# Kernel tuning notes

Hardware: AMD Instinct MI355X
Metric: run time of the kernel (lower is better)

## Reference

```python
import jax, jax.numpy as jnp
import numpy as np

NODE_DIM, HIDDEN_DIM, OUT_DIM = 64, 128, 64
N_NODES, N_EDGES = 50000, 800000
SLOPE = 0.05


def leaky(x):
    return jnp.where(x >= 0, x, SLOPE * x)


def setup_inputs() -> dict:
    key = jax.random.key(0)
    ks = jax.random.split(key, 8)
    x = jax.random.normal(ks[0], (N_NODES, NODE_DIM), dtype=jnp.float32)
    edge_index = jax.random.randint(ks[1], (2, N_EDGES), 0, N_NODES, dtype=jnp.int64)
    s0 = 1.0 / np.sqrt(NODE_DIM)
    s1 = 1.0 / np.sqrt(HIDDEN_DIM)
    W0 = jax.random.uniform(ks[2], (NODE_DIM, HIDDEN_DIM), jnp.float32, -s0, s0)
    b0 = jax.random.uniform(ks[3], (HIDDEN_DIM,), jnp.float32, -s0, s0)
    W1 = jax.random.uniform(ks[4], (HIDDEN_DIM, HIDDEN_DIM), jnp.float32, -s1, s1)
    b1 = jax.random.uniform(ks[5], (HIDDEN_DIM,), jnp.float32, -s1, s1)
    W2 = jax.random.uniform(ks[6], (HIDDEN_DIM, OUT_DIM), jnp.float32, -s1, s1)
    b2 = jax.random.uniform(ks[7], (OUT_DIM,), jnp.float32, -s1, s1)
    return {"x": x, "edge_index": edge_index, "W0": W0, "b0": b0,
            "W1": W1, "b1": b1, "W2": W2, "b2": b2}


def reference(x, edge_index, W0, b0, W1, b1, W2, b2):
    # gather-sum: [E, node_dim]
    e = x[edge_index[0]] + x[edge_index[1]]
    h = leaky(e @ W0 + b0)          # [E, hidden]
    h = leaky(h @ W1 + b1)          # [E, hidden]
    out = leaky(h @ W2 + b2)        # [E, out]
    return out
```

## Files before the change

kernel.cpp:

```cpp
#include <hip/hip_runtime.h>

typedef _Float16 half8  __attribute__((ext_vector_type(8)));
typedef float    floatx4 __attribute__((ext_vector_type(4)));

#define N_NODES 50000
#define N_EDGES 800000
#define SLOPE 0.05f

#define WS_XH  0ull
#define WS_W0  (WS_XH + (size_t)N_NODES * 64 * 2)
#define WS_W1  (WS_W0 + 128 * 64 * 2)
#define WS_W2  (WS_W1 + 128 * 128 * 2)
#define WS_B0  (WS_W2 + 64 * 128 * 2)
#define WS_B1  (WS_B0 + 128 * 4)
#define WS_B2  (WS_B1 + 128 * 4)

#define HC_STRIDE 40
#define XCONV_BLOCKS 782
#define PREP_BLOCKS (XCONV_BLOCKS + 65)

__device__ __forceinline__ float leaky(float t) { return t >= 0.f ? t : SLOPE * t; }

__global__ void prep_kernel(const float* __restrict__ x,
                            const float* __restrict__ W0, const float* __restrict__ W1,
                            const float* __restrict__ W2, const float* __restrict__ b0,
                            const float* __restrict__ b1, const float* __restrict__ b2,
                            unsigned char* __restrict__ ws) {
    const int b = blockIdx.x;
    if (b < XCONV_BLOCKS) {
        _Float16* xh = (_Float16*)(ws + WS_XH);
        const int i = (b * 512 + threadIdx.x) * 8;
        if (i < N_NODES * 64) {
            floatx4 u0 = *(const floatx4*)(x + i);
            floatx4 u1 = *(const floatx4*)(x + i + 4);
            half8 h;
            #pragma unroll
            for (int j = 0; j < 4; ++j) { h[j] = (_Float16)u0[j]; h[4 + j] = (_Float16)u1[j]; }
            *(half8*)(xh + i) = h;
        }
        return;
    }
    const int t = (b - XCONV_BLOCKS) * 512 + threadIdx.x;
    _Float16* w0t = (_Float16*)(ws + WS_W0);
    _Float16* wt1 = (_Float16*)(ws + WS_W1);
    _Float16* wt2 = (_Float16*)(ws + WS_W2);
    if (t < 8192) {
        int k = t >> 7, n = t & 127;
        w0t[n * 64 + k] = (_Float16)W0[k * 128 + n];
    } else if (t < 24576) {
        int i2 = t - 8192, k = i2 >> 7, n = i2 & 127;
        wt1[n * 128 + k] = (_Float16)W1[k * 128 + n];
    } else if (t < 32768) {
        int i2 = t - 24576, k = i2 >> 6, n = i2 & 63;
        wt2[n * 128 + k] = (_Float16)W2[k * 64 + n];
    } else if (t < 33088) {
        int i2 = t - 32768;
        if (i2 < 128) ((float*)(ws + WS_B0))[i2] = b0[i2];
        else if (i2 < 256) ((float*)(ws + WS_B1))[i2 - 128] = b1[i2 - 128];
        else ((float*)(ws + WS_B2))[i2 - 256] = b2[i2 - 256];
    }
}

__global__ __launch_bounds__(512, 4) void edge_kernel(const int* __restrict__ ei,
                                                      const unsigned char* __restrict__ ws,
                                                      float* __restrict__ out) {
    __shared__ __align__(16) _Float16 w0s[128 * 64];
    __shared__ __align__(16) _Float16 w1s[128 * 128];
    __shared__ __align__(16) _Float16 w2s[64 * 128];
    __shared__ __align__(16) _Float16 hc[8][16 * HC_STRIDE];
    __shared__ __align__(16) float b0s[128], b1s[128], b2s[64];

    const _Float16* __restrict__ xh  = (const _Float16*)(ws + WS_XH);
    const _Float16* __restrict__ w0g = (const _Float16*)(ws + WS_W0);
    const _Float16* __restrict__ w1g = (const _Float16*)(ws + WS_W1);
    const _Float16* __restrict__ w2g = (const _Float16*)(ws + WS_W2);

    const int wave = threadIdx.x >> 6, lane = threadIdx.x & 63;
    const int cl = lane & 15, q = lane >> 4;
    const int base = blockIdx.x * 256 + wave * 32;

    const int r0 = base + cl;
    const int s0 = ei[r0], d0 = ei[N_EDGES + r0];
    const int s1 = ei[r0 + 16], d1 = ei[N_EDGES + r0 + 16];

    const _Float16* ps0 = xh + (size_t)s0 * 64 + q * 8;
    const _Float16* pd0 = xh + (size_t)d0 * 64 + q * 8;
    const _Float16* ps1 = xh + (size_t)s1 * 64 + q * 8;
    const _Float16* pd1 = xh + (size_t)d1 * 64 + q * 8;
    half8 us00 = *(const half8*)(ps0);  half8 us01 = *(const half8*)(ps0 + 32);
    half8 ud00 = *(const half8*)(pd0);  half8 ud01 = *(const half8*)(pd0 + 32);
    half8 us10 = *(const half8*)(ps1);  half8 us11 = *(const half8*)(ps1 + 32);
    half8 ud10 = *(const half8*)(pd1);  half8 ud11 = *(const half8*)(pd1 + 32);

    {
        const int t = threadIdx.x;
        #pragma unroll
        for (int it = 0; it < 4; ++it) {
            int c = t + it * 512, row = c >> 4, cc = c & 15;
            int dst = (row * 128 + cc * 8) ^ ((row & 7) << 3);
            *(half8*)&w1s[dst] = *(const half8*)&w1g[row * 128 + cc * 8];
        }
        #pragma unroll
        for (int it = 0; it < 2; ++it) {
            int c = t + it * 512, row = c >> 4, cc = c & 15;
            int dst = (row * 128 + cc * 8) ^ ((row & 7) << 3);
            *(half8*)&w2s[dst] = *(const half8*)&w2g[row * 128 + cc * 8];
        }
        #pragma unroll
        for (int it = 0; it < 2; ++it) {
            int c = t + it * 512, row = c >> 3, cc = c & 7;
            int dst = (row * 64 + cc * 8) ^ ((row & 7) << 3);
            *(half8*)&w0s[dst] = *(const half8*)&w0g[row * 64 + cc * 8];
        }
        if (t < 128) { b0s[t] = *(const float*)(ws + WS_B0 + t * 4);
                       b1s[t] = *(const float*)(ws + WS_B1 + t * 4); }
        else if (t < 192) b2s[t - 128] = *(const float*)(ws + WS_B2 + (size_t)(t - 128) * 4);
    }
    __syncthreads();

    half8 a0[2][2];
    a0[0][0] = us00 + ud00;  a0[0][1] = us01 + ud01;
    a0[1][0] = us10 + ud10;  a0[1][1] = us11 + ud11;

    const int swz = (cl & 7) << 3;
    _Float16* hw = &hc[wave][0];

    half8 a1[2][4];
    #pragma unroll
    for (int kk = 0; kk < 4; ++kk) {
        const int nA = 2 * kk, nB = 2 * kk + 1;
        half8 wA0 = *(const half8*)&w0s[((nA * 16 + cl) * 64 + q * 8) ^ swz];
        half8 wA1 = *(const half8*)&w0s[((nA * 16 + cl) * 64 + 32 + q * 8) ^ swz];
        half8 wB0 = *(const half8*)&w0s[((nB * 16 + cl) * 64 + q * 8) ^ swz];
        half8 wB1 = *(const half8*)&w0s[((nB * 16 + cl) * 64 + 32 + q * 8) ^ swz];
        const float bbA = b0s[nA * 16 + cl], bbB = b0s[nB * 16 + cl];
        #pragma unroll
        for (int g = 0; g < 2; ++g) {
            floatx4 cA = {0.f, 0.f, 0.f, 0.f}, cB = {0.f, 0.f, 0.f, 0.f};
            cA = __builtin_amdgcn_mfma_f32_16x16x32_f16(a0[g][0], wA0, cA, 0, 0, 0);
            cA = __builtin_amdgcn_mfma_f32_16x16x32_f16(a0[g][1], wA1, cA, 0, 0, 0);
            cB = __builtin_amdgcn_mfma_f32_16x16x32_f16(a0[g][0], wB0, cB, 0, 0, 0);
            cB = __builtin_amdgcn_mfma_f32_16x16x32_f16(a0[g][1], wB1, cB, 0, 0, 0);
            #pragma unroll
            for (int rr = 0; rr < 4; ++rr) {
                hw[(q * 4 + rr) * HC_STRIDE + cl]      = (_Float16)leaky(cA[rr] + bbA);
                hw[(q * 4 + rr) * HC_STRIDE + 16 + cl] = (_Float16)leaky(cB[rr] + bbB);
            }
            a1[g][kk] = *(const half8*)&hw[cl * HC_STRIDE + q * 8];
        }
    }

    floatx4 acc2[2][4];
    #pragma unroll
    for (int g = 0; g < 2; ++g)
        #pragma unroll
        for (int n2 = 0; n2 < 4; ++n2) acc2[g][n2] = (floatx4){0.f, 0.f, 0.f, 0.f};

    #pragma unroll
    for (int ks = 0; ks < 4; ++ks) {
        const int nA = 2 * ks, nB = 2 * ks + 1;
        floatx4 cA0 = {0.f,0.f,0.f,0.f}, cA1 = {0.f,0.f,0.f,0.f};
        floatx4 cB0 = {0.f,0.f,0.f,0.f}, cB1 = {0.f,0.f,0.f,0.f};
        #pragma unroll
        for (int kk = 0; kk < 4; ++kk) {
            half8 b = *(const half8*)&w1s[((nA * 16 + cl) * 128 + kk * 32 + q * 8) ^ swz];
            cA0 = __builtin_amdgcn_mfma_f32_16x16x32_f16(a1[0][kk], b, cA0, 0, 0, 0);
            cA1 = __builtin_amdgcn_mfma_f32_16x16x32_f16(a1[1][kk], b, cA1, 0, 0, 0);
        }
        #pragma unroll
        for (int kk = 0; kk < 4; ++kk) {
            half8 b = *(const half8*)&w1s[((nB * 16 + cl) * 128 + kk * 32 + q * 8) ^ swz];
            cB0 = __builtin_amdgcn_mfma_f32_16x16x32_f16(a1[0][kk], b, cB0, 0, 0, 0);
            cB1 = __builtin_amdgcn_mfma_f32_16x16x32_f16(a1[1][kk], b, cB1, 0, 0, 0);
        }
        const float bbA = b1s[nA * 16 + cl], bbB = b1s[nB * 16 + cl];
        half8 a2[2];
        #pragma unroll
        for (int g = 0; g < 2; ++g) {
            const floatx4 cc0 = g ? cA1 : cA0;
            const floatx4 cc1 = g ? cB1 : cB0;
            #pragma unroll
            for (int rr = 0; rr < 4; ++rr) {
                hw[(q * 4 + rr) * HC_STRIDE + cl]      = (_Float16)leaky(cc0[rr] + bbA);
                hw[(q * 4 + rr) * HC_STRIDE + 16 + cl] = (_Float16)leaky(cc1[rr] + bbB);
            }
            a2[g] = *(const half8*)&hw[cl * HC_STRIDE + q * 8];
        }
        #pragma unroll
        for (int n2 = 0; n2 < 4; ++n2) {
            half8 b = *(const half8*)&w2s[((n2 * 16 + cl) * 128 + ks * 32 + q * 8) ^ swz];
            acc2[0][n2] = __builtin_amdgcn_mfma_f32_16x16x32_f16(b, a2[0], acc2[0][n2], 0, 0, 0);
            acc2[1][n2] = __builtin_amdgcn_mfma_f32_16x16x32_f16(b, a2[1], acc2[1][n2], 0, 0, 0);
        }
    }

    #pragma unroll
    for (int n2 = 0; n2 < 4; ++n2) {
        floatx4 bb = *(const floatx4*)&b2s[n2 * 16 + q * 4];
        #pragma unroll
        for (int g = 0; g < 2; ++g) {
            floatx4 o;
            #pragma unroll
            for (int rr = 0; rr < 4; ++rr) o[rr] = leaky(acc2[g][n2][rr] + bb[rr]);
            *(floatx4*)(out + (size_t)(base + g * 16 + cl) * 64 + n2 * 16 + q * 4) = o;
        }
    }
}

extern "C" void kernel_launch(void* const* d_in, const int* in_sizes, int n_in,
                              void* d_out, int out_size, void* d_ws, size_t ws_size,
                              hipStream_t stream) {
    const float* x  = (const float*)d_in[0];
    const int*   ei = (const int*)d_in[1];
    const float* W0 = (const float*)d_in[2];
    const float* b0 = (const float*)d_in[3];
    const float* W1 = (const float*)d_in[4];
    const float* b1 = (const float*)d_in[5];
    const float* W2 = (const float*)d_in[6];
    const float* b2 = (const float*)d_in[7];
    float* out = (float*)d_out;
    unsigned char* ws = (unsigned char*)d_ws;

    prep_kernel<<<PREP_BLOCKS, 512, 0, stream>>>(x, W0, W1, W2, b0, b1, b2, ws);
    edge_kernel<<<N_EDGES / 256, 512, 0, stream>>>(ei, ws, out);
}
```

Baseline: 276.1 us.

## Process two edge tiles per block and prefetch second tile's gathers

Each block now handles 512 edges instead of 256, which halves the number of blocks that each reload the full fp16 weight set into LDS. The second tile's node-feature gathers are issued before the first tile's MLP runs, so their latency can overlap with the MFMA work. The cost is extra registers held for the prefetched data (t1[8]), which may reduce occupancy under the existing launch bounds. Fewer blocks also means less parallelism per CU.

Measured after the change: 334.7 us. 21.2% more time.

```diff
diff --git a/kernel.cpp b/kernel.cpp
--- a/kernel.cpp
+++ b/kernel.cpp
@@ -18,6 +18,7 @@
 #define HC_STRIDE 40
 #define XCONV_BLOCKS 782
 #define PREP_BLOCKS (XCONV_BLOCKS + 65)
+#define EDGE_BLOCKS 1563
 
 __device__ __forceinline__ float leaky(float t) { return t >= 0.f ? t : SLOPE * t; }
 
@@ -61,6 +62,94 @@
     }
 }
 
+__device__ __forceinline__ void mlp_tile(const half8 a0[2][2], const int base,
+        const _Float16* __restrict__ w0s, const _Float16* __restrict__ w1s,
+        const _Float16* __restrict__ w2s, _Float16* __restrict__ hw,
+        const float* __restrict__ b0s, const float* __restrict__ b1s,
+        const float* __restrict__ b2s, float* __restrict__ out,
+        const int cl, const int q, const int swz) {
+    half8 a1[2][4];
+    #pragma unroll
+    for (int kk = 0; kk < 4; ++kk) {
+        const int nA = 2 * kk, nB = 2 * kk + 1;
+        half8 wA0 = *(const half8*)&w0s[((nA * 16 + cl) * 64 + q * 8) ^ swz];
+        half8 wA1 = *(const half8*)&w0s[((nA * 16 + cl) * 64 + 32 + q * 8) ^ swz];
+        half8 wB0 = *(const half8*)&w0s[((nB * 16 + cl) * 64 + q * 8) ^ swz];
+        half8 wB1 = *(const half8*)&w0s[((nB * 16 + cl) * 64 + 32 + q * 8) ^ swz];
+        const float bbA = b0s[nA * 16 + cl], bbB = b0s[nB * 16 + cl];
+        #pragma unroll
+        for (int g = 0; g < 2; ++g) {
+            floatx4 cA = {0.f, 0.f, 0.f, 0.f}, cB = {0.f, 0.f, 0.f, 0.f};
+            cA = __builtin_amdgcn_mfma_f32_16x16x32_f16(a0[g][0], wA0, cA, 0, 0, 0);
+            cA = __builtin_amdgcn_mfma_f32_16x16x32_f16(a0[g][1], wA1, cA, 0, 0, 0);
+            cB = __builtin_amdgcn_mfma_f32_16x16x32_f16(a0[g][0], wB0, cB, 0, 0, 0);
+            cB = __builtin_amdgcn_mfma_f32_16x16x32_f16(a0[g][1], wB1, cB, 0, 0, 0);
+            #pragma unroll
+            for (int rr = 0; rr < 4; ++rr) {
+                hw[(q * 4 + rr) * HC_STRIDE + cl]      = (_Float16)leaky(cA[rr] + bbA);
+                hw[(q * 4 + rr) * HC_STRIDE + 16 + cl] = (_Float16)leaky(cB[rr] + bbB);
+            }
+            a1[g][kk] = *(const half8*)&hw[cl * HC_STRIDE + q * 8];
+        }
+    }
+
+    floatx4 acc2[2][4];
+    #pragma unroll
+    for (int g = 0; g < 2; ++g)
+        #pragma unroll
+        for (int n2 = 0; n2 < 4; ++n2) acc2[g][n2] = (floatx4){0.f, 0.f, 0.f, 0.f};
+
+    #pragma unroll
+    for (int ks = 0; ks < 4; ++ks) {
+        const int nA = 2 * ks, nB = 2 * ks + 1;
+        floatx4 cA0 = {0.f,0.f,0.f,0.f}, cA1 = {0.f,0.f,0.f,0.f};
+        floatx4 cB0 = {0.f,0.f,0.f,0.f}, cB1 = {0.f,0.f,0.f,0.f};
+        #pragma unroll
+        for (int kk = 0; kk < 4; ++kk) {
+            half8 b = *(const half8*)&w1s[((nA * 16 + cl) * 128 + kk * 32 + q * 8) ^ swz];
+            cA0 = __builtin_amdgcn_mfma_f32_16x16x32_f16(a1[0][kk], b, cA0, 0, 0, 0);
+            cA1 = __builtin_amdgcn_mfma_f32_16x16x32_f16(a1[1][kk], b, cA1, 0, 0, 0);
+        }
+        #pragma unroll
+        for (int kk = 0; kk < 4; ++kk) {
+            half8 b = *(const half8*)&w1s[((nB * 16 + cl) * 128 + kk * 32 + q * 8) ^ swz];
+            cB0 = __builtin_amdgcn_mfma_f32_16x16x32_f16(a1[0][kk], b, cB0, 0, 0, 0);
+            cB1 = __builtin_amdgcn_mfma_f32_16x16x32_f16(a1[1][kk], b, cB1, 0, 0, 0);
+        }
+        const float bbA = b1s[nA * 16 + cl], bbB = b1s[nB * 16 + cl];
+        half8 a2[2];
+        #pragma unroll
+        for (int g = 0; g < 2; ++g) {
+            const floatx4 cc0 = g ? cA1 : cA0;
+            const floatx4 cc1 = g ? cB1 : cB0;
+            #pragma unroll
+            for (int rr = 0; rr < 4; ++rr) {
+                hw[(q * 4 + rr) * HC_STRIDE + cl]      = (_Float16)leaky(cc0[rr] + bbA);
+                hw[(q * 4 + rr) * HC_STRIDE + 16 + cl] = (_Float16)leaky(cc1[rr] + bbB);
+            }
+            a2[g] = *(const half8*)&hw[cl * HC_STRIDE + q * 8];
+        }
+        #pragma unroll
+        for (int n2 = 0; n2 < 4; ++n2) {
+            half8 b = *(const half8*)&w2s[((n2 * 16 + cl) * 128 + ks * 32 + q * 8) ^ swz];
+            acc2[0][n2] = __builtin_amdgcn_mfma_f32_16x16x32_f16(b, a2[0], acc2[0][n2], 0, 0, 0);
+            acc2[1][n2] = __builtin_amdgcn_mfma_f32_16x16x32_f16(b, a2[1], acc2[1][n2], 0, 0, 0);
+        }
+    }
+
+    #pragma unroll
+    for (int n2 = 0; n2 < 4; ++n2) {
+        floatx4 bb = *(const floatx4*)&b2s[n2 * 16 + q * 4];
+        #pragma unroll
+        for (int g = 0; g < 2; ++g) {
+            floatx4 o;
+            #pragma unroll
+            for (int rr = 0; rr < 4; ++rr) o[rr] = leaky(acc2[g][n2][rr] + bb[rr]);
+            *(floatx4*)(out + (size_t)(base + g * 16 + cl) * 64 + n2 * 16 + q * 4) = o;
+        }
+    }
+}
+
 __global__ __launch_bounds__(512, 4) void edge_kernel(const int* __restrict__ ei,
                                                       const unsigned char* __restrict__ ws,
                                                       float* __restrict__ out) {
@@ -77,16 +166,25 @@
 
     const int wave = threadIdx.x >> 6, lane = threadIdx.x & 63;
     const int cl = lane & 15, q = lane >> 4;
-    const int base = blockIdx.x * 256 + wave * 32;
-
-    const int r0 = base + cl;
-    const int s0 = ei[r0], d0 = ei[N_EDGES + r0];
-    const int s1 = ei[r0 + 16], d1 = ei[N_EDGES + r0 + 16];
-
-    const _Float16* ps0 = xh + (size_t)s0 * 64 + q * 8;
-    const _Float16* pd0 = xh + (size_t)d0 * 64 + q * 8;
-    const _Float16* ps1 = xh + (size_t)s1 * 64 + q * 8;
-    const _Float16* pd1 = xh + (size_t)d1 * 64 + q * 8;
+    const int tbase = blockIdx.x * 512;
+    const bool has1 = (tbase + 256) < N_EDGES;
+    const int base0 = tbase + wave * 32;
+    const int base1 = tbase + 256 + wave * 32;
+
+    const int r0 = base0 + cl;
+    const int s00 = ei[r0], d00 = ei[N_EDGES + r0];
+    const int s01 = ei[r0 + 16], d01 = ei[N_EDGES + r0 + 16];
+    int s10 = 0, d10 = 0, s11 = 0, d11 = 0;
+    if (has1) {
+        const int r1 = base1 + cl;
+        s10 = ei[r1]; d10 = ei[N_EDGES + r1];
+        s11 = ei[r1 + 16]; d11 = ei[N_EDGES + r1 + 16];
+    }
+
+    const _Float16* ps0 = xh + (size_t)s00 * 64 + q * 8;
+    const _Float16* pd0 = xh + (size_t)d00 * 64 + q * 8;
+    const _Float16* ps1 = xh + (size_t)s01 * 64 + q * 8;
+    const _Float16* pd1 = xh + (size_t)d01 * 64 + q * 8;
     half8 us00 = *(const half8*)(ps0);  half8 us01 = *(const half8*)(ps0 + 32);
     half8 ud00 = *(const half8*)(pd0);  half8 ud01 = *(const half8*)(pd0 + 32);
     half8 us10 = *(const half8*)(ps1);  half8 us11 = *(const half8*)(ps1 + 32);
@@ -122,88 +220,28 @@
     a0[0][0] = us00 + ud00;  a0[0][1] = us01 + ud01;
     a0[1][0] = us10 + ud10;  a0[1][1] = us11 + ud11;
 
+    half8 t1[8];
+    if (has1) {
+        const _Float16* qs0 = xh + (size_t)s10 * 64 + q * 8;
+        const _Float16* qd0 = xh + (size_t)d10 * 64 + q * 8;
+        const _Float16* qs1 = xh + (size_t)s11 * 64 + q * 8;
+        const _Float16* qd1 = xh + (size_t)d11 * 64 + q * 8;
+        t1[0] = *(const half8*)(qs0);  t1[1] = *(const half8*)(qs0 + 32);
+        t1[2] = *(const half8*)(qd0);  t1[3] = *(const half8*)(qd0 + 32);
+        t1[4] = *(const half8*)(qs1);  t1[5] = *(const half8*)(qs1 + 32);
+        t1[6] = *(const half8*)(qd1);  t1[7] = *(const half8*)(qd1 + 32);
+    }
+
     const int swz = (cl & 7) << 3;
     _Float16* hw = &hc[wave][0];
 
-    half8 a1[2][4];
-    #pragma unroll
-    for (int kk = 0; kk < 4; ++kk) {
-        const int nA = 2 * kk, nB = 2 * kk + 1;
-        half8 wA0 = *(const half8*)&w0s[((nA * 16 + cl) * 64 + q * 8) ^ swz];
-        half8 wA1 = *(const half8*)&w0s[((nA * 16 + cl) * 64 + 32 + q * 8) ^ swz];
-        half8 wB0 = *(const half8*)&w0s[((nB * 16 + cl) * 64 + q * 8) ^ swz];
-        half8 wB1 = *(const half8*)&w0s[((nB * 16 + cl) * 64 + 32 + q * 8) ^ swz];
-        const float bbA = b0s[nA * 16 + cl], bbB = b0s[nB * 16 + cl];
-        #pragma unroll
-        for (int g = 0; g < 2; ++g) {
-            floatx4 cA = {0.f, 0.f, 0.f, 0.f}, cB = {0.f, 0.f, 0.f, 0.f};
-            cA = __builtin_amdgcn_mfma_f32_16x16x32_f16(a0[g][0], wA0, cA, 0, 0, 0);
-            cA = __builtin_amdgcn_mfma_f32_16x16x32_f16(a0[g][1], wA1, cA, 0, 0, 0);
-            cB = __builtin_amdgcn_mfma_f32_16x16x32_f16(a0[g][0], wB0, cB, 0, 0, 0);
-            cB = __builtin_amdgcn_mfma_f32_16x16x32_f16(a0[g][1], wB1, cB, 0, 0, 0);
-            #pragma unroll
-            for (int rr = 0; rr < 4; ++rr) {
-                hw[(q * 4 + rr) * HC_STRIDE + cl]      = (_Float16)leaky(cA[rr] + bbA);
-                hw[(q * 4 + rr) * HC_STRIDE + 16 + cl] = (_Float16)leaky(cB[rr] + bbB);
-            }
-            a1[g][kk] = *(const half8*)&hw[cl * HC_STRIDE + q * 8];
-        }
-    }
-
-    floatx4 acc2[2][4];
-    #pragma unroll
-    for (int g = 0; g < 2; ++g)
-        #pragma unroll
-        for (int n2 = 0; n2 < 4; ++n2) acc2[g][n2] = (floatx4){0.f, 0.f, 0.f, 0.f};
-
-    #pragma unroll
-    for (int ks = 0; ks < 4; ++ks) {
-        const int nA = 2 * ks, nB = 2 * ks + 1;
-        floatx4 cA0 = {0.f,0.f,0.f,0.f}, cA1 = {0.f,0.f,0.f,0.f};
-        floatx4 cB0 = {0.f,0.f,0.f,0.f}, cB1 = {0.f,0.f,0.f,0.f};
-        #pragma unroll
-        for (int kk = 0; kk < 4; ++kk) {
-            half8 b = *(const half8*)&w1s[((nA * 16 + cl) * 128 + kk * 32 + q * 8) ^ swz];
-            cA0 = __builtin_amdgcn_mfma_f32_16x16x32_f16(a1[0][kk], b, cA0, 0, 0, 0);
-            cA1 = __builtin_amdgcn_mfma_f32_16x16x32_f16(a1[1][kk], b, cA1, 0, 0, 0);
-        }
-        #pragma unroll
-        for (int kk = 0; kk < 4; ++kk) {
-            half8 b = *(const half8*)&w1s[((nB * 16 + cl) * 128 + kk * 32 + q * 8) ^ swz];
-            cB0 = __builtin_amdgcn_mfma_f32_16x16x32_f16(a1[0][kk], b, cB0, 0, 0, 0);
-            cB1 = __builtin_amdgcn_mfma_f32_16x16x32_f16(a1[1][kk], b, cB1, 0, 0, 0);
-        }
-        const float bbA = b1s[nA * 16 + cl], bbB = b1s[nB * 16 + cl];
-        half8 a2[2];
-        #pragma unroll
-        for (int g = 0; g < 2; ++g) {
-            const floatx4 cc0 = g ? cA1 : cA0;
-            const floatx4 cc1 = g ? cB1 : cB0;
-            #pragma unroll
-            for (int rr = 0; rr < 4; ++rr) {
-                hw[(q * 4 + rr) * HC_STRIDE + cl]      = (_Float16)leaky(cc0[rr] + bbA);
-                hw[(q * 4 + rr) * HC_STRIDE + 16 + cl] = (_Float16)leaky(cc1[rr] + bbB);
-            }
-            a2[g] = *(const half8*)&hw[cl * HC_STRIDE + q * 8];
-        }
-        #pragma unroll
-        for (int n2 = 0; n2 < 4; ++n2) {
-            half8 b = *(const half8*)&w2s[((n2 * 16 + cl) * 128 + ks * 32 + q * 8) ^ swz];
-            acc2[0][n2] = __builtin_amdgcn_mfma_f32_16x16x32_f16(b, a2[0], acc2[0][n2], 0, 0, 0);
-            acc2[1][n2] = __builtin_amdgcn_mfma_f32_16x16x32_f16(b, a2[1], acc2[1][n2], 0, 0, 0);
-        }
-    }
-
-    #pragma unroll
-    for (int n2 = 0; n2 < 4; ++n2) {
-        floatx4 bb = *(const floatx4*)&b2s[n2 * 16 + q * 4];
-        #pragma unroll
-        for (int g = 0; g < 2; ++g) {
-            floatx4 o;
-            #pragma unroll
-            for (int rr = 0; rr < 4; ++rr) o[rr] = leaky(acc2[g][n2][rr] + bb[rr]);
-            *(floatx4*)(out + (size_t)(base + g * 16 + cl) * 64 + n2 * 16 + q * 4) = o;
-        }
+    mlp_tile(a0, base0, w0s, w1s, w2s, hw, b0s, b1s, b2s, out, cl, q, swz);
+
+    if (has1) {
+        half8 a0b[2][2];
+        a0b[0][0] = t1[0] + t1[2];  a0b[0][1] = t1[1] + t1[3];
+        a0b[1][0] = t1[4] + t1[6];  a0b[1][1] = t1[5] + t1[7];
+        mlp_tile(a0b, base1, w0s, w1s, w2s, hw, b0s, b1s, b2s, out, cl, q, swz);
     }
 }
 
@@ -222,5 +260,5 @@
     unsigned char* ws = (unsigned char*)d_ws;
 
     prep_kernel<<<PREP_BLOCKS, 512, 0, stream>>>(x, W0, W1, W2, b0, b1, b2, ws);
-    edge_kernel<<<N_EDGES / 256, 512, 0, stream>>>(ei, ws, out);
-}
+    edge_kernel<<<EDGE_BLOCKS, 512, 0, stream>>>(ei, ws, out);
+}
```
